# Kernel tuning notes

Measured on AMD Instinct MI355X. Metric: run time of the kernel, lower is better.

The kernel has to match this reference:

```python
import jax, jax.numpy as jnp
import numpy as np

NUM_Q = 500000
NUM_E = 250000
DIM = 256
HEADS = 4
NEG_SLOPE = 0.01
EPS = 1e-16


def setup_inputs() -> dict:
    key = jax.random.key(0)
    k1, k2, k3, k4, k5 = jax.random.split(key, 5)
    x_q = jax.random.normal(k1, (NUM_Q, DIM), dtype=jnp.float32)
    x_edge = jax.random.normal(k2, (NUM_E, DIM), dtype=jnp.float32)
    edge_ids = jax.random.randint(k3, (NUM_Q,), 0, NUM_E, dtype=jnp.int64)
    # learned params: w_q (input_dim, output_dim), attention weight (H, 2*dim/H)
    w_q = jax.random.normal(k4, (DIM, DIM), dtype=jnp.float32) / np.sqrt(DIM)
    weight = jax.random.normal(k5, (HEADS, 2 * DIM // HEADS), dtype=jnp.float32) / np.sqrt(2 * DIM // HEADS)
    return {"x_q": x_q, "x_edge": x_edge, "w_q": w_q, "weight": weight, "edge_ids": edge_ids}


def reference(x_q, x_edge, w_q, weight, edge_ids):
    nq = x_q.shape[0]
    ne = x_edge.shape[0]
    h = weight.shape[0]
    # project qualifier pairs: (nq, dim) -> (nq, H, d_head)
    xq = (x_q @ w_q).reshape(nq, h, -1)
    # gather edge reps per qualifier pair: (nq, H, d_head)
    xe = x_edge[edge_ids].reshape(nq, h, -1)
    # per-head attention logits: eh
    alpha = jnp.einsum('ehd,hd->eh', jnp.concatenate([xe, xq], axis=-1), weight)
    alpha = jax.nn.leaky_relu(alpha, NEG_SLOPE)
    # segment softmax grouped by edge_ids (numerically stable)
    seg_max = jax.ops.segment_max(alpha, edge_ids, num_segments=ne)
    seg_max = jnp.where(jnp.isfinite(seg_max), seg_max, 0.0)  # empty segments
    ex = jnp.exp(alpha - seg_max[edge_ids])
    seg_sum = jax.ops.segment_sum(ex, edge_ids, num_segments=ne)
    alpha = ex / (seg_sum[edge_ids] + EPS)
    # weight qualifier reps and scatter-add to edges
    xq = (alpha[..., None] * xq).reshape(nq, -1)
    return jax.ops.segment_sum(xq, edge_ids, num_segments=ne)
```

## Files before the change

### kernel.cpp

```cpp
#include <hip/hip_runtime.h>
#include <hip/hip_bf16.h>

#define DIM 256
#define HEADS 4
#define NEG_SLOPE 0.01f

typedef unsigned short u16;
typedef __attribute__((ext_vector_type(8))) short short8;
typedef __attribute__((ext_vector_type(4))) float f32x4;
typedef __attribute__((ext_vector_type(4))) unsigned short u16x4;

__device__ __forceinline__ u16 f2bf(float f) {
    unsigned u = __float_as_uint(f);
    unsigned r = (u + 0x7fffu + ((u >> 16) & 1u)) >> 16;
    return (u16)r;
}
__device__ __forceinline__ float bf2f(u16 h) {
    return __uint_as_float(((unsigned)h) << 16);
}

__global__ __launch_bounds__(256) void prepb_kernel(const float* __restrict__ B,
                                                    u16* __restrict__ BThi) {
    int k = blockIdx.x;
    int n = threadIdx.x;
    BThi[n * 256 + k] = f2bf(B[k * 256 + n]);
}

__global__ __launch_bounds__(256) void beta_kernel(const float* __restrict__ xe,
                                                   const float* __restrict__ weight,
                                                   float* __restrict__ beta, int NE) {
    int wid = blockIdx.x * 4 + (threadIdx.x >> 6);
    if (wid >= NE) return;
    int lane = threadIdx.x & 63;
    int h = lane >> 4;
    float4 v = *reinterpret_cast<const float4*>(xe + (size_t)wid * DIM + lane * 4);
    float4 w = *reinterpret_cast<const float4*>(weight + h * 128 + (lane & 15) * 4);
    float p = v.x * w.x + v.y * w.y + v.z * w.z + v.w * w.w;
    p += __shfl_xor(p, 1);
    p += __shfl_xor(p, 2);
    p += __shfl_xor(p, 4);
    p += __shfl_xor(p, 8);
    if ((lane & 15) == 0) beta[(size_t)wid * 4 + h] = p;
}

__global__ __launch_bounds__(256, 3) void gemm_fused_kernel(const float* __restrict__ A,
                                                            const u16* __restrict__ BThi,
                                                            const float* __restrict__ weight,
                                                            const float* __restrict__ beta,
                                                            const int* __restrict__ eids,
                                                            u16* __restrict__ xq_out,
                                                            float* __restrict__ exv,
                                                            float* __restrict__ segsum,
                                                            unsigned* __restrict__ counts,
                                                            int NQ) {
    __shared__ u16 A_s[2][64 * 32];

    const int t = threadIdx.x;
    const int lane = t & 63;
    const int wc = t >> 6;
    const int lr = lane & 15;
    const int kg = lane >> 4;
    const long brow = (long)blockIdx.x * 64;

    const int s_row0 = t >> 3, s_c4 = t & 7;
    const float* aptr0;
    const float* aptr1;
    {
        long g0 = brow + s_row0;       if (g0 >= NQ) g0 = NQ - 1;
        long g1 = brow + s_row0 + 32;  if (g1 >= NQ) g1 = NQ - 1;
        aptr0 = A + g0 * DIM + s_c4 * 4;
        aptr1 = A + g1 * DIM + s_c4 * 4;
    }
    const u16* brows[4];
#pragma unroll
    for (int n = 0; n < 4; ++n)
        brows[n] = BThi + (wc * 64 + n * 16 + lr) * 256 + kg * 8;

    f32x4 acc[4][4];
#pragma unroll
    for (int m = 0; m < 4; ++m)
#pragma unroll
        for (int n = 0; n < 4; ++n) acc[m][n] = (f32x4){0.f, 0.f, 0.f, 0.f};

    float4 a_reg0, a_reg1;
    auto load_a = [&](int k0) {
        a_reg0 = *reinterpret_cast<const float4*>(aptr0 + k0);
        a_reg1 = *reinterpret_cast<const float4*>(aptr1 + k0);
    };
    auto write_a = [&](int buf) {
#pragma unroll
        for (int i = 0; i < 2; ++i) {
            int row = s_row0 + i * 32;
            float4 v = i ? a_reg1 : a_reg0;
            u16x4 hv;
            hv.x = f2bf(v.x); hv.y = f2bf(v.y); hv.z = f2bf(v.z); hv.w = f2bf(v.w);
            int swz = (s_c4 >> 1) ^ (row & 3) ^ ((row >> 2) & 3);
            int off = row * 32 + (swz << 3) + ((s_c4 & 1) << 2);
            *reinterpret_cast<u16x4*>(&A_s[buf][off]) = hv;
        }
    };

    load_a(0);
    write_a(0);
    __syncthreads();

    for (int step = 0; step < 8; ++step) {
        const int buf = step & 1;
        const int k0 = step * 32;
        if (step < 7) load_a(k0 + 32);

        short8 bh[4];
#pragma unroll
        for (int n = 0; n < 4; ++n)
            bh[n] = *reinterpret_cast<const short8*>(brows[n] + k0);

#pragma unroll
        for (int m = 0; m < 4; ++m) {
            int rr = m * 16 + lr;
            int off = rr * 32 + ((kg ^ (rr & 3) ^ ((rr >> 2) & 3)) << 3);
            short8 ah = *reinterpret_cast<const short8*>(&A_s[buf][off]);
#pragma unroll
            for (int n = 0; n < 4; ++n)
                acc[m][n] = __builtin_amdgcn_mfma_f32_16x16x32_bf16(ah, bh[n], acc[m][n], 0, 0, 0);
        }

        if (step < 7) {
            write_a(buf ^ 1);
            __syncthreads();
        }
    }

    float wv[4];
#pragma unroll
    for (int n = 0; n < 4; ++n) wv[n] = weight[wc * 128 + 64 + n * 16 + lr];

#pragma unroll
    for (int m = 0; m < 4; ++m) {
#pragma unroll
        for (int r = 0; r < 4; ++r) {
            long row = brow + m * 16 + kg * 4 + r;
            bool ok = row < NQ;
            float p = 0.f;
#pragma unroll
            for (int n = 0; n < 4; ++n) {
                float v = acc[m][n][r];
                if (ok) xq_out[row * DIM + wc * 64 + n * 16 + lr] = f2bf(v);
                p = fmaf(v, wv[n], p);
            }
            p += __shfl_xor(p, 1);
            p += __shfl_xor(p, 2);
            p += __shfl_xor(p, 4);
            p += __shfl_xor(p, 8);
            if (ok && lr == 0) {
                int j = eids[row];
                float l = beta[(size_t)j * 4 + wc] + p;
                l = l > 0.f ? l : NEG_SLOPE * l;
                float e = __expf(l);
                exv[row * 4 + wc] = e;
                atomicAdd(&segsum[(size_t)j * 4 + wc], e);
                if (wc == 0) atomicAdd(&counts[j], 1u);
            }
        }
    }
}

__global__ __launch_bounds__(256) void scan1_kernel(const unsigned* __restrict__ counts,
                                                    unsigned* __restrict__ offs,
                                                    unsigned* __restrict__ blocksums, int NE) {
    __shared__ unsigned s[256];
    int t = threadIdx.x;
    int base = blockIdx.x * 1024 + t * 4;
    unsigned v[4], sum = 0;
#pragma unroll
    for (int i = 0; i < 4; ++i) {
        v[i] = (base + i < NE) ? counts[base + i] : 0u;
        sum += v[i];
    }
    s[t] = sum;
    __syncthreads();
    for (int off = 1; off < 256; off <<= 1) {
        unsigned y = (t >= off) ? s[t - off] : 0u;
        __syncthreads();
        s[t] += y;
        __syncthreads();
    }
    unsigned excl = s[t] - sum;
#pragma unroll
    for (int i = 0; i < 4; ++i) {
        if (base + i < NE) offs[base + i] = excl;
        excl += v[i];
    }
    if (t == 255) blocksums[blockIdx.x] = s[255];
}

__global__ __launch_bounds__(256) void scan2_kernel(unsigned* __restrict__ blocksums, int NB) {
    __shared__ unsigned s[256];
    int t = threadIdx.x;
    unsigned v = (t < NB) ? blocksums[t] : 0u;
    s[t] = v;
    __syncthreads();
    for (int off = 1; off < 256; off <<= 1) {
        unsigned y = (t >= off) ? s[t - off] : 0u;
        __syncthreads();
        s[t] += y;
        __syncthreads();
    }
    if (t < NB) blocksums[t] = s[t] - v;
}

__global__ __launch_bounds__(256) void scan3_kernel(unsigned* __restrict__ offs,
                                                    const unsigned* __restrict__ blocksums,
                                                    unsigned* __restrict__ cursor, int NE) {
    int t = threadIdx.x;
    int base = blockIdx.x * 1024 + t * 4;
    unsigned add = blocksums[blockIdx.x];
#pragma unroll
    for (int i = 0; i < 4; ++i) {
        if (base + i < NE) {
            unsigned o = offs[base + i] + add;
            offs[base + i] = o;
            cursor[base + i] = o;
        }
    }
}

__global__ __launch_bounds__(256) void fill_kernel(const int* __restrict__ eids,
                                                   unsigned* __restrict__ cursor,
                                                   int* __restrict__ qlist, int NQ) {
    int e = blockIdx.x * blockDim.x + threadIdx.x;
    if (e >= NQ) return;
    int j = eids[e];
    unsigned pos = atomicAdd(&cursor[j], 1u);
    qlist[pos] = e;
}

__global__ __launch_bounds__(256) void gather_kernel(const float* __restrict__ exv,
                                                     const float* __restrict__ segsum,
                                                     const unsigned* __restrict__ offs,
                                                     const unsigned* __restrict__ counts,
                                                     const int* __restrict__ qlist,
                                                     const u16* __restrict__ xq,
                                                     float* __restrict__ out, int NE) {
    int j = blockIdx.x * 4 + (threadIdx.x >> 6);
    if (j >= NE) return;
    int lane = threadIdx.x & 63;
    int h = lane >> 4;
    unsigned beg = offs[j];
    unsigned n = counts[j];
    float inv = 1.0f / (segsum[(size_t)j * 4 + h] + 1e-16f);
    float4 a0 = make_float4(0.f, 0.f, 0.f, 0.f);
    float4 a1 = make_float4(0.f, 0.f, 0.f, 0.f);
    unsigned i = 0;
    for (; i + 2 <= n; i += 2) {
        int q0 = qlist[beg + i];
        int q1 = qlist[beg + i + 1];
        float w0 = exv[(size_t)q0 * 4 + h] * inv;
        float w1 = exv[(size_t)q1 * 4 + h] * inv;
        u16x4 v0 = *reinterpret_cast<const u16x4*>(xq + (size_t)q0 * DIM + lane * 4);
        u16x4 v1 = *reinterpret_cast<const u16x4*>(xq + (size_t)q1 * DIM + lane * 4);
        a0.x = fmaf(w0, bf2f(v0.x), a0.x); a1.x = fmaf(w1, bf2f(v1.x), a1.x);
        a0.y = fmaf(w0, bf2f(v0.y), a0.y); a1.y = fmaf(w1, bf2f(v1.y), a1.y);
        a0.z = fmaf(w0, bf2f(v0.z), a0.z); a1.z = fmaf(w1, bf2f(v1.z), a1.z);
        a0.w = fmaf(w0, bf2f(v0.w), a0.w); a1.w = fmaf(w1, bf2f(v1.w), a1.w);
    }
    if (i < n) {
        int q0 = qlist[beg + i];
        float w0 = exv[(size_t)q0 * 4 + h] * inv;
        u16x4 v0 = *reinterpret_cast<const u16x4*>(xq + (size_t)q0 * DIM + lane * 4);
        a0.x = fmaf(w0, bf2f(v0.x), a0.x);
        a0.y = fmaf(w0, bf2f(v0.y), a0.y);
        a0.z = fmaf(w0, bf2f(v0.z), a0.z);
        a0.w = fmaf(w0, bf2f(v0.w), a0.w);
    }
    float4 acc = make_float4(a0.x + a1.x, a0.y + a1.y, a0.z + a1.z, a0.w + a1.w);
    *reinterpret_cast<float4*>(out + (size_t)j * DIM + lane * 4) = acc;
}

extern "C" void kernel_launch(void* const* d_in, const int* in_sizes, int n_in,
                              void* d_out, int out_size, void* d_ws, size_t ws_size,
                              hipStream_t stream) {
    (void)n_in; (void)out_size; (void)ws_size;
    const float* x_q    = (const float*)d_in[0];
    const float* x_edge = (const float*)d_in[1];
    const float* w_q    = (const float*)d_in[2];
    const float* weight = (const float*)d_in[3];
    const int*   eids   = (const int*)d_in[4];
    const int NQ = in_sizes[0] / DIM;
    const int NE = in_sizes[1] / DIM;
    float* out = (float*)d_out;

    u16*      xq        = (u16*)d_ws;
    float*    exv       = (float*)(xq + (size_t)NQ * DIM);
    float*    beta      = exv + (size_t)NQ * 4;
    float*    segsum    = beta + (size_t)NE * 4;
    unsigned* counts    = (unsigned*)(segsum + (size_t)NE * 4);
    unsigned* offs      = counts + NE;
    unsigned* cursor    = offs + NE;
    int*      qlist     = (int*)(cursor + NE);
    unsigned* blocksums = (unsigned*)(qlist + NQ);
    u16*      BThi      = (u16*)(blocksums + 256);

    const int NB = (NE + 1023) / 1024;

    hipMemsetAsync(segsum, 0, (size_t)NE * 4 * sizeof(float), stream);
    hipMemsetAsync(counts, 0, (size_t)NE * sizeof(unsigned), stream);

    prepb_kernel<<<256, 256, 0, stream>>>(w_q, BThi);
    beta_kernel<<<(NE + 3) / 4, 256, 0, stream>>>(x_edge, weight, beta, NE);
    gemm_fused_kernel<<<(NQ + 63) / 64, 256, 0, stream>>>(x_q, BThi, weight, beta, eids,
                                                          xq, exv, segsum, counts, NQ);
    scan1_kernel<<<NB, 256, 0, stream>>>(counts, offs, blocksums, NE);
    scan2_kernel<<<1, 256, 0, stream>>>(blocksums, NB);
    scan3_kernel<<<NB, 256, 0, stream>>>(offs, blocksums, cursor, NE);
    fill_kernel<<<(NQ + 255) / 256, 256, 0, stream>>>(eids, cursor, qlist, NQ);
    gather_kernel<<<(NE + 3) / 4, 256, 0, stream>>>(exv, segsum, offs, counts, qlist, xq, out, NE);
}
```

Before: 561.9 us.

## Restructure GEMM main loop into two-stage register/LDS pipeline with packed bf16 conversion

Measured after the change: 600.4 us. 6.9% more time.

```diff
diff --git a/kernel.cpp b/kernel.cpp
--- a/kernel.cpp
+++ b/kernel.cpp
@@ -17,6 +17,12 @@
 }
 __device__ __forceinline__ float bf2f(u16 h) {
     return __uint_as_float(((unsigned)h) << 16);
+}
+__device__ __forceinline__ unsigned cvt2(float a, float b) {
+    __hip_bfloat162 h = __float22bfloat162_rn(make_float2(a, b));
+    unsigned u;
+    __builtin_memcpy(&u, &h, 4);
+    return u;
 }
 
 __global__ __launch_bounds__(256) void prepb_kernel(const float* __restrict__ B,
@@ -53,7 +59,8 @@
                                                             float* __restrict__ segsum,
                                                             unsigned* __restrict__ counts,
                                                             int NQ) {
-    __shared__ u16 A_s[2][64 * 32];
+    __shared__ u16 A_s0[64 * 32];
+    __shared__ u16 A_s1[64 * 32];
 
     const int t = threadIdx.x;
     const int lane = t & 63;
@@ -71,61 +78,95 @@
         aptr0 = A + g0 * DIM + s_c4 * 4;
         aptr1 = A + g1 * DIM + s_c4 * 4;
     }
+    const int off_w0 = s_row0 * 32 + ((((s_c4 >> 1) ^ (s_row0 & 3) ^ ((s_row0 >> 2) & 3))) << 3) + ((s_c4 & 1) << 2);
+    const int s_row1 = s_row0 + 32;
+    const int off_w1 = s_row1 * 32 + ((((s_c4 >> 1) ^ (s_row1 & 3) ^ ((s_row1 >> 2) & 3))) << 3) + ((s_c4 & 1) << 2);
+
     const u16* brows[4];
 #pragma unroll
     for (int n = 0; n < 4; ++n)
         brows[n] = BThi + (wc * 64 + n * 16 + lr) * 256 + kg * 8;
 
+    int rdoff[4];
+#pragma unroll
+    for (int m = 0; m < 4; ++m) {
+        int rr = m * 16 + lr;
+        rdoff[m] = rr * 32 + ((kg ^ (rr & 3) ^ ((rr >> 2) & 3)) << 3);
+    }
+
     f32x4 acc[4][4];
 #pragma unroll
     for (int m = 0; m < 4; ++m)
 #pragma unroll
         for (int n = 0; n < 4; ++n) acc[m][n] = (f32x4){0.f, 0.f, 0.f, 0.f};
 
-    float4 a_reg0, a_reg1;
-    auto load_a = [&](int k0) {
-        a_reg0 = *reinterpret_cast<const float4*>(aptr0 + k0);
-        a_reg1 = *reinterpret_cast<const float4*>(aptr1 + k0);
-    };
-    auto write_a = [&](int buf) {
-#pragma unroll
-        for (int i = 0; i < 2; ++i) {
-            int row = s_row0 + i * 32;
-            float4 v = i ? a_reg1 : a_reg0;
-            u16x4 hv;
-            hv.x = f2bf(v.x); hv.y = f2bf(v.y); hv.z = f2bf(v.z); hv.w = f2bf(v.w);
-            int swz = (s_c4 >> 1) ^ (row & 3) ^ ((row >> 2) & 3);
-            int off = row * 32 + (swz << 3) + ((s_c4 & 1) << 2);
-            *reinterpret_cast<u16x4*>(&A_s[buf][off]) = hv;
-        }
-    };
-
-    load_a(0);
-    write_a(0);
+    float4 aP0, aP1, aQ0, aQ1;
+    short8 bhP[4], bhQ[4];
+
+#pragma unroll
+    for (int n = 0; n < 4; ++n)
+        bhP[n] = *reinterpret_cast<const short8*>(brows[n] + 0);
+    aP0 = *reinterpret_cast<const float4*>(aptr0 + 0);
+    aP1 = *reinterpret_cast<const float4*>(aptr1 + 0);
+    aQ0 = *reinterpret_cast<const float4*>(aptr0 + 32);
+    aQ1 = *reinterpret_cast<const float4*>(aptr1 + 32);
+    {
+        uint2 w0 = make_uint2(cvt2(aP0.x, aP0.y), cvt2(aP0.z, aP0.w));
+        uint2 w1 = make_uint2(cvt2(aP1.x, aP1.y), cvt2(aP1.z, aP1.w));
+        *reinterpret_cast<uint2*>(&A_s0[off_w0]) = w0;
+        *reinterpret_cast<uint2*>(&A_s1[0]) = *reinterpret_cast<uint2*>(&A_s1[0]);
+        *reinterpret_cast<uint2*>(&A_s0[off_w1]) = w1;
+    }
     __syncthreads();
 
-    for (int step = 0; step < 8; ++step) {
-        const int buf = step & 1;
-        const int k0 = step * 32;
-        if (step < 7) load_a(k0 + 32);
-
-        short8 bh[4];
+#pragma unroll 1
+    for (int it = 0; it < 4; ++it) {
+        const bool more = it < 3;
+        const int s = 2 * it;
+
 #pragma unroll
         for (int n = 0; n < 4; ++n)
-            bh[n] = *reinterpret_cast<const short8*>(brows[n] + k0);
-
+            bhQ[n] = *reinterpret_cast<const short8*>(brows[n] + (s + 1) * 32);
+        if (more) {
+            aP0 = *reinterpret_cast<const float4*>(aptr0 + (s + 2) * 32);
+            aP1 = *reinterpret_cast<const float4*>(aptr1 + (s + 2) * 32);
+        }
 #pragma unroll
         for (int m = 0; m < 4; ++m) {
-            int rr = m * 16 + lr;
-            int off = rr * 32 + ((kg ^ (rr & 3) ^ ((rr >> 2) & 3)) << 3);
-            short8 ah = *reinterpret_cast<const short8*>(&A_s[buf][off]);
+            short8 ah = *reinterpret_cast<const short8*>(&A_s0[rdoff[m]]);
 #pragma unroll
             for (int n = 0; n < 4; ++n)
-                acc[m][n] = __builtin_amdgcn_mfma_f32_16x16x32_bf16(ah, bh[n], acc[m][n], 0, 0, 0);
-        }
-
-        if (step < 7) {
-            write_a(buf ^ 1);
+                acc[m][n] = __builtin_amdgcn_mfma_f32_16x16x32_bf16(ah, bhP[n], acc[m][n], 0, 0, 0);
+        }
+        {
+            uint2 w0 = make_uint2(cvt2(aQ0.x, aQ0.y), cvt2(aQ0.z, aQ0.w));
+            uint2 w1 = make_uint2(cvt2(aQ1.x, aQ1.y), cvt2(aQ1.z, aQ1.w));
+            __syncthreads();
+            *reinterpret_cast<uint2*>(&A_s1[off_w0]) = w0;
+            *reinterpret_cast<uint2*>(&A_s1[off_w1]) = w1;
+            __syncthreads();
+        }
+
+        if (more) {
+#pragma unroll
+            for (int n = 0; n < 4; ++n)
+                bhP[n] = *reinterpret_cast<const short8*>(brows[n] + (s + 2) * 32);
+            aQ0 = *reinterpret_cast<const float4*>(aptr0 + (s + 3) * 32);
+            aQ1 = *reinterpret_cast<const float4*>(aptr1 + (s + 3) * 32);
+        }
+#pragma unroll
+        for (int m = 0; m < 4; ++m) {
+            short8 ah = *reinterpret_cast<const short8*>(&A_s1[rdoff[m]]);
+#pragma unroll
+            for (int n = 0; n < 4; ++n)
+                acc[m][n] = __builtin_amdgcn_mfma_f32_16x16x32_bf16(ah, bhQ[n], acc[m][n], 0, 0, 0);
+        }
+        if (more) {
+            uint2 w0 = make_uint2(cvt2(aP0.x, aP0.y), cvt2(aP0.z, aP0.w));
+            uint2 w1 = make_uint2(cvt2(aP1.x, aP1.y), cvt2(aP1.z, aP1.w));
+            __syncthreads();
+            *reinterpret_cast<uint2*>(&A_s0[off_w0]) = w0;
+            *reinterpret_cast<uint2*>(&A_s0[off_w1]) = w1;
             __syncthreads();
         }
     }
```

## Deepen A-tile prefetch to three register stages in projection GEMM

Applied to the files above, without the earlier changes.

Result: slower. 584.2 us (+4.0%).

```diff
diff --git a/kernel.cpp b/kernel.cpp
--- a/kernel.cpp
+++ b/kernel.cpp
@@ -17,6 +17,12 @@
 }
 __device__ __forceinline__ float bf2f(u16 h) {
     return __uint_as_float(((unsigned)h) << 16);
+}
+__device__ __forceinline__ unsigned cvt2(float a, float b) {
+    __hip_bfloat162 h = __float22bfloat162_rn(make_float2(a, b));
+    unsigned u;
+    __builtin_memcpy(&u, &h, 4);
+    return u;
 }
 
 __global__ __launch_bounds__(256) void prepb_kernel(const float* __restrict__ B,
@@ -71,62 +77,74 @@
         aptr0 = A + g0 * DIM + s_c4 * 4;
         aptr1 = A + g1 * DIM + s_c4 * 4;
     }
+    const int off_w0 = s_row0 * 32 + ((((s_c4 >> 1) ^ (s_row0 & 3) ^ ((s_row0 >> 2) & 3))) << 3) + ((s_c4 & 1) << 2);
+    const int s_row1 = s_row0 + 32;
+    const int off_w1 = s_row1 * 32 + ((((s_c4 >> 1) ^ (s_row1 & 3) ^ ((s_row1 >> 2) & 3))) << 3) + ((s_c4 & 1) << 2);
+
     const u16* brows[4];
 #pragma unroll
     for (int n = 0; n < 4; ++n)
         brows[n] = BThi + (wc * 64 + n * 16 + lr) * 256 + kg * 8;
 
+    int rdoff[4];
+#pragma unroll
+    for (int m = 0; m < 4; ++m) {
+        int rr = m * 16 + lr;
+        rdoff[m] = rr * 32 + ((kg ^ (rr & 3) ^ ((rr >> 2) & 3)) << 3);
+    }
+
     f32x4 acc[4][4];
 #pragma unroll
     for (int m = 0; m < 4; ++m)
 #pragma unroll
         for (int n = 0; n < 4; ++n) acc[m][n] = (f32x4){0.f, 0.f, 0.f, 0.f};
 
-    float4 a_reg0, a_reg1;
-    auto load_a = [&](int k0) {
-        a_reg0 = *reinterpret_cast<const float4*>(aptr0 + k0);
-        a_reg1 = *reinterpret_cast<const float4*>(aptr1 + k0);
-    };
-    auto write_a = [&](int buf) {
-#pragma unroll
-        for (int i = 0; i < 2; ++i) {
-            int row = s_row0 + i * 32;
-            float4 v = i ? a_reg1 : a_reg0;
-            u16x4 hv;
-            hv.x = f2bf(v.x); hv.y = f2bf(v.y); hv.z = f2bf(v.z); hv.w = f2bf(v.w);
-            int swz = (s_c4 >> 1) ^ (row & 3) ^ ((row >> 2) & 3);
-            int off = row * 32 + (swz << 3) + ((s_c4 & 1) << 2);
-            *reinterpret_cast<u16x4*>(&A_s[buf][off]) = hv;
-        }
-    };
-
-    load_a(0);
-    write_a(0);
-    __syncthreads();
-
-    for (int step = 0; step < 8; ++step) {
-        const int buf = step & 1;
-        const int k0 = step * 32;
-        if (step < 7) load_a(k0 + 32);
-
-        short8 bh[4];
-#pragma unroll
-        for (int n = 0; n < 4; ++n)
-            bh[n] = *reinterpret_cast<const short8*>(brows[n] + k0);
-
+    float4 areg[3][2];
+
+#pragma unroll
+    for (int s0 = 0; s0 < 3; ++s0) {
+        areg[s0][0] = *reinterpret_cast<const float4*>(aptr0 + s0 * 32);
+        areg[s0][1] = *reinterpret_cast<const float4*>(aptr1 + s0 * 32);
+    }
+    {
+        uint2 w0 = make_uint2(cvt2(areg[0][0].x, areg[0][0].y), cvt2(areg[0][0].z, areg[0][0].w));
+        uint2 w1 = make_uint2(cvt2(areg[0][1].x, areg[0][1].y), cvt2(areg[0][1].z, areg[0][1].w));
+        *reinterpret_cast<uint2*>(&A_s[0][off_w0]) = w0;
+        *reinterpret_cast<uint2*>(&A_s[0][off_w1]) = w1;
+    }
+    asm volatile("s_waitcnt lgkmcnt(0)" ::: "memory");
+    __builtin_amdgcn_s_barrier();
+
+#pragma unroll
+    for (int s = 0; s < 8; ++s) {
+        const int buf = s & 1;
+        if (s < 7) {
+            const int set = (s + 1) % 3;
+            uint2 w0 = make_uint2(cvt2(areg[set][0].x, areg[set][0].y), cvt2(areg[set][0].z, areg[set][0].w));
+            uint2 w1 = make_uint2(cvt2(areg[set][1].x, areg[set][1].y), cvt2(areg[set][1].z, areg[set][1].w));
+            *reinterpret_cast<uint2*>(&A_s[buf ^ 1][off_w0]) = w0;
+            *reinterpret_cast<uint2*>(&A_s[buf ^ 1][off_w1]) = w1;
+        }
+        short8 bh0 = *reinterpret_cast<const short8*>(brows[0] + s * 32);
+        short8 bh1 = *reinterpret_cast<const short8*>(brows[1] + s * 32);
+        short8 bh2 = *reinterpret_cast<const short8*>(brows[2] + s * 32);
+        short8 bh3 = *reinterpret_cast<const short8*>(brows[3] + s * 32);
+        if (s < 5) {
+            const int set = s % 3;
+            areg[set][0] = *reinterpret_cast<const float4*>(aptr0 + (s + 3) * 32);
+            areg[set][1] = *reinterpret_cast<const float4*>(aptr1 + (s + 3) * 32);
+        }
 #pragma unroll
         for (int m = 0; m < 4; ++m) {
-            int rr = m * 16 + lr;
-            int off = rr * 32 + ((kg ^ (rr & 3) ^ ((rr >> 2) & 3)) << 3);
-            short8 ah = *reinterpret_cast<const short8*>(&A_s[buf][off]);
-#pragma unroll
-            for (int n = 0; n < 4; ++n)
-                acc[m][n] = __builtin_amdgcn_mfma_f32_16x16x32_bf16(ah, bh[n], acc[m][n], 0, 0, 0);
-        }
-
-        if (step < 7) {
-            write_a(buf ^ 1);
-            __syncthreads();
+            short8 ah = *reinterpret_cast<const short8*>(&A_s[buf][rdoff[m]]);
+            acc[m][0] = __builtin_amdgcn_mfma_f32_16x16x32_bf16(ah, bh0, acc[m][0], 0, 0, 0);
+            acc[m][1] = __builtin_amdgcn_mfma_f32_16x16x32_bf16(ah, bh1, acc[m][1], 0, 0, 0);
+            acc[m][2] = __builtin_amdgcn_mfma_f32_16x16x32_bf16(ah, bh2, acc[m][2], 0, 0, 0);
+            acc[m][3] = __builtin_amdgcn_mfma_f32_16x16x32_bf16(ah, bh3, acc[m][3], 0, 0, 0);
+        }
+        if (s < 7) {
+            asm volatile("s_waitcnt lgkmcnt(0)" ::: "memory");
+            __builtin_amdgcn_s_barrier();
         }
     }
 
```
